# Kernel tuning notes

Measured on AMD Instinct MI355X. Metric: run time of the kernel, lower is better.

Reference implementation:

```python
import jax, jax.numpy as jnp
import numpy as np

DIM = 4096
NH = 32
NKV = 8
HD = DIM // NH          # 128
REP = NH // NKV          # 4
B = 1
T = 2048
THETA = 500000.0
NEG = -1e9


def setup_inputs() -> dict:
    key = jax.random.key(0)
    ks = jax.random.split(key, 6)
    x = jax.random.normal(ks[0], (B, T, DIM), jnp.float32)
    # RoPE tables (real/imag parts of freqs_cis = exp(i * t * inv_freq))
    inv_freq = 1.0 / (THETA ** (np.arange(0, HD, 2, dtype=np.float32) / HD))  # (HD/2,)
    ang = np.outer(np.arange(T, dtype=np.float32), inv_freq)                  # (T, HD/2)
    freqs_cos = jnp.asarray(np.cos(ang), jnp.float32)
    freqs_sin = jnp.asarray(np.sin(ang), jnp.float32)
    # additive causal mask for prefill (pos=0): (T, T)
    mask = jnp.where(np.tril(np.ones((T, T), dtype=bool)), 0.0, NEG).astype(jnp.float32)
    cache_k = jnp.zeros((B, T, NKV, HD), jnp.float32)
    cache_v = jnp.zeros((B, T, NKV, HD), jnp.float32)
    s = 0.02
    wk_w = jax.random.normal(ks[1], (NKV * HD, DIM), jnp.float32) * s
    wk_b = jnp.zeros((NKV * HD,), jnp.float32)
    wv_w = jax.random.normal(ks[2], (NKV * HD, DIM), jnp.float32) * s
    wv_b = jnp.zeros((NKV * HD,), jnp.float32)
    wo_w = jax.random.normal(ks[3], (DIM, DIM), jnp.float32) * s
    wo_b = jnp.zeros((DIM,), jnp.float32)
    return dict(x=x, freqs_cos=freqs_cos, freqs_sin=freqs_sin, mask=mask,
                cache_k=cache_k, cache_v=cache_v,
                wk_w=wk_w, wk_b=wk_b, wv_w=wv_w, wv_b=wv_b,
                wo_w=wo_w, wo_b=wo_b, pos=0)


def _rope(t, cos, sin):
    # t: (B, T, H, HD); pairs (even, odd) form complex numbers
    tr = t.reshape(*t.shape[:-1], HD // 2, 2)
    re, im = tr[..., 0], tr[..., 1]
    c = cos[None, :, None, :]
    s = sin[None, :, None, :]
    out = jnp.stack([re * c - im * s, re * s + im * c], axis=-1)
    return out.reshape(t.shape)


def reference(x, freqs_cos, freqs_sin, mask, cache_k, cache_v,
              wk_w, wk_b, wv_w, wv_b, wo_w, wo_b, pos):
    Bx, Tx, D = x.shape
    # NOTE: faithful to source bug -- q projection uses wo (shared with output proj)
    q = x @ wo_w.T + wo_b                        # (B, T, D)
    k = x @ wk_w.T + wk_b                        # (B, T, NKV*HD)
    v = x @ wv_w.T + wv_b
    q = q.reshape(Bx, Tx, NH, HD)
    k = k.reshape(Bx, Tx, NKV, HD)
    v = v.reshape(Bx, Tx, NKV, HD)
    q = _rope(q, freqs_cos, freqs_sin)
    k = _rope(k, freqs_cos, freqs_sin)
    # KV-cache append then read back [:pos+T]
    ck = cache_k.at[:Bx, pos:pos + Tx].set(k)
    cv = cache_v.at[:Bx, pos:pos + Tx].set(v)
    k = ck[:Bx, :pos + Tx]
    v = cv[:Bx, :pos + Tx]
    # repeat_kv (GQA expansion)
    k = jnp.repeat(k, REP, axis=2)               # (B, S, NH, HD)
    v = jnp.repeat(v, REP, axis=2)
    scale = 1.0 / jnp.sqrt(jnp.float32(HD))
    scores = jnp.einsum('bqhd,bkhd->bhqk', q, k) * scale
    scores = scores + mask[None, None, :, :]
    p = jax.nn.softmax(scores.astype(jnp.float32), axis=-1)
    out = jnp.einsum('bhqk,bkhd->bqhd', p, v).reshape(Bx, Tx, D)
    return out @ wo_w.T + wo_b
```

## Files before the change

kernel.cpp:

```cpp
#include <hip/hip_runtime.h>
#include <stdint.h>
#include <stddef.h>

#define T_SEQ 2048
#define DIM   4096
#define NH    32
#define NKV   8
#define HD    128
#define KVD   (NKV*HD)

typedef __attribute__((ext_vector_type(8))) short short8;
typedef __attribute__((ext_vector_type(4))) float floatx4;

static __device__ __forceinline__ float bf2f(short u) {
    union { unsigned int i; float f; } c; c.i = ((unsigned int)(unsigned short)u) << 16; return c.f;
}
static __device__ __forceinline__ short f2bf(float f) {
    union { float f; unsigned int u; } c; c.f = f;
    unsigned int r = c.u + 0x7fff + ((c.u >> 16) & 1);
    return (short)(r >> 16);
}
static __device__ __forceinline__ short8 ld8_f2b(const float* p) {
    floatx4 a = *(const floatx4*)p;
    floatx4 b = *(const floatx4*)(p + 4);
    short8 r;
    r[0]=f2bf(a[0]); r[1]=f2bf(a[1]); r[2]=f2bf(a[2]); r[3]=f2bf(a[3]);
    r[4]=f2bf(b[0]); r[5]=f2bf(b[1]); r[6]=f2bf(b[2]); r[7]=f2bf(b[3]);
    return r;
}

#define GLD16(g, l) __builtin_amdgcn_global_load_lds( \
    (const __attribute__((address_space(1))) unsigned int*)(g), \
    (__attribute__((address_space(3))) unsigned int*)(l), 16, 0, 0)

template<int CTRL>
static __device__ __forceinline__ float dppf(float x) {
    return __int_as_float(__builtin_amdgcn_update_dpp(
        0, __float_as_int(x), CTRL, 0xf, 0xf, true));
}
static __device__ __forceinline__ float rowmax16(float x) {
    x = fmaxf(x, dppf<0xB1>(x));
    x = fmaxf(x, dppf<0x4E>(x));
    x = fmaxf(x, dppf<0x141>(x));
    x = fmaxf(x, dppf<0x140>(x));
    return x;
}
static __device__ __forceinline__ float rowsum16(float x) {
    x += dppf<0xB1>(x);
    x += dppf<0x4E>(x);
    x += dppf<0x141>(x);
    x += dppf<0x140>(x);
    return x;
}

__global__ __launch_bounds__(256)
void cvt_bf16(const float* __restrict__ x, const float* __restrict__ wk,
              const float* __restrict__ wv, const float* __restrict__ wo,
              short* __restrict__ xb, short* __restrict__ wkb,
              short* __restrict__ wvb, short* __restrict__ wob) {
    size_t i8 = ((size_t)blockIdx.x * 256 + threadIdx.x) * 8;
    const float* src; short* dst; size_t off;
    if (i8 < 8388608)        { src = x;  dst = xb;  off = i8; }
    else if (i8 < 12582912)  { src = wk; dst = wkb; off = i8 - 8388608; }
    else if (i8 < 16777216)  { src = wv; dst = wvb; off = i8 - 12582912; }
    else                     { src = wo; dst = wob; off = i8 - 16777216; }
    *(short8*)(dst + off) = ld8_f2b(src + off);
}

template<bool C_F32>
static __device__ __forceinline__
void gemm_core(const short* __restrict__ A, const short* __restrict__ B,
               const float* __restrict__ bias, void* __restrict__ Cp,
               int N, int K, int bm, int bn) {
    __shared__ short sA0[128*32];
    __shared__ short sA1[128*32];
    __shared__ short sB0[128*32];
    __shared__ short sB1[128*32];
    const int tid  = threadIdx.x;
    const int wave = tid >> 6, lane = tid & 63;
    const int l15  = lane & 15, lq = lane >> 4;
    const int wm   = (wave >> 1) * 64, wn = (wave & 1) * 64;

    floatx4 acc[4][4];
    #pragma unroll
    for (int i = 0; i < 4; i++)
        #pragma unroll
        for (int j = 0; j < 4; j++)
            acc[i][j] = (floatx4)(0.0f);

    const int c0 = tid, c1 = 256 + tid;
    const int r0 = c0 >> 2, k0 = (c0 & 3) * 8;
    const int r1 = c1 >> 2, k1 = (c1 & 3) * 8;
    const short* pA0 = A + (size_t)(bm + r0) * K + k0;
    const short* pA1 = A + (size_t)(bm + r1) * K + k1;
    const short* pB0 = B + (size_t)(bn + r0) * K + k0;
    const short* pB1 = B + (size_t)(bn + r1) * K + k1;

    auto stage = [&](short* dA, short* dB, int kt) {
        GLD16(pA0 + kt, dA + c0 * 8);
        GLD16(pA1 + kt, dA + c1 * 8);
        GLD16(pB0 + kt, dB + c0 * 8);
        GLD16(pB1 + kt, dB + c1 * 8);
    };
    auto compute = [&](const short* dA, const short* dB) {
        short8 af[4], bfr[4];
        #pragma unroll
        for (int mi = 0; mi < 4; mi++)
            af[mi] = *(const short8*)&dA[(wm + mi*16 + l15)*32 + lq*8];
        #pragma unroll
        for (int ni = 0; ni < 4; ni++)
            bfr[ni] = *(const short8*)&dB[(wn + ni*16 + l15)*32 + lq*8];
        #pragma unroll
        for (int mi = 0; mi < 4; mi++)
            #pragma unroll
            for (int ni = 0; ni < 4; ni++)
                acc[mi][ni] = __builtin_amdgcn_mfma_f32_16x16x32_bf16(af[mi], bfr[ni], acc[mi][ni], 0, 0, 0);
    };

    stage(sA0, sB0, 0);
    __syncthreads();

    const int nt = K >> 5;
    for (int t = 0; t < nt; t += 2) {
        stage(sA1, sB1, (t + 1) * 32);
        compute(sA0, sB0);
        __syncthreads();
        if (t + 2 < nt) stage(sA0, sB0, (t + 2) * 32);
        compute(sA1, sB1);
        __syncthreads();
    }

    #pragma unroll
    for (int ni = 0; ni < 4; ni++) {
        int col = bn + wn + ni*16 + l15;
        float bv = bias[col];
        #pragma unroll
        for (int mi = 0; mi < 4; mi++) {
            int row = bm + wm + mi*16 + lq*4;
            #pragma unroll
            for (int r = 0; r < 4; r++) {
                float v = acc[mi][ni][r] + bv;
                if (C_F32) ((float*)Cp)[(size_t)(row + r)*N + col] = v;
                else       ((short*)Cp)[(size_t)(row + r)*N + col] = f2bf(v);
            }
        }
    }
}

template<bool C_F32>
__global__ __launch_bounds__(256)
void gemm_bt(const short* __restrict__ A, const short* __restrict__ B,
             const float* __restrict__ bias, void* __restrict__ Cp,
             int N, int K) {
    gemm_core<C_F32>(A, B, bias, Cp, N, K, blockIdx.y * 128, blockIdx.x * 128);
}

__global__ __launch_bounds__(256)
void gemm_kv(const short* __restrict__ A,
             const short* __restrict__ Bk, const float* __restrict__ bk, short* __restrict__ Ck,
             const short* __restrict__ Bv, const float* __restrict__ bv, short* __restrict__ Cv) {
    const short* B = blockIdx.z ? Bv : Bk;
    const float* bias = blockIdx.z ? bv : bk;
    short* C = blockIdx.z ? Cv : Ck;
    gemm_core<false>(A, B, bias, C, KVD, DIM, blockIdx.y * 128, blockIdx.x * 128);
}

__global__ __launch_bounds__(256)
void rope_k(short* __restrict__ Q, short* __restrict__ Kc,
            const float* __restrict__ fc, const float* __restrict__ fs) {
    int idx = blockIdx.x * 256 + threadIdx.x;
    const int NQ = T_SEQ * NH  * (HD/2);
    const int NK = T_SEQ * NKV * (HD/2);
    short* base; int t, i; size_t off;
    if (idx < NQ) {
        i = idx & 63;
        int th = idx >> 6;
        t = th >> 5;
        off = (size_t)th * HD + i*2;
        base = Q;
    } else if (idx < NQ + NK) {
        int kidx = idx - NQ;
        i = kidx & 63;
        int th = kidx >> 6;
        t = th >> 3;
        off = (size_t)th * HD + i*2;
        base = Kc;
    } else return;
    float re = bf2f(base[off]), im = bf2f(base[off+1]);
    float c = fc[t*64 + i], s = fs[t*64 + i];
    base[off]   = f2bf(re*c - im*s);
    base[off+1] = f2bf(re*s + im*c);
}

__global__ __launch_bounds__(256)
void vtrans(const short* __restrict__ V, short* __restrict__ Vt) {
    __shared__ short sT[64*72];
    const int tid = threadIdx.x;
    const int bt = blockIdx.x, bd = blockIdx.y;
    #pragma unroll
    for (int i = 0; i < 2; i++) {
        int c = i*256 + tid;
        int r = c >> 3, c8 = (c & 7) * 8;
        *(short8*)&sT[r*72 + c8] = *(const short8*)(V + (size_t)(bt*64 + r)*KVD + bd*64 + c8);
    }
    __syncthreads();
    #pragma unroll
    for (int i = 0; i < 2; i++) {
        int c = i*256 + tid;
        int d = c >> 3, t8 = (c & 7) * 8;
        short8 o;
        #pragma unroll
        for (int j = 0; j < 8; j++) o[j] = sT[(t8 + j)*72 + d];
        *(short8*)(Vt + (size_t)(bd*64 + d)*T_SEQ + bt*64 + t8) = o;
    }
}

#define ROWK 136
#define ROWV 72

__global__ __launch_bounds__(256, 2)
void flash_attn(const short* __restrict__ Q, const short* __restrict__ Kc,
                const short* __restrict__ Vt, short* __restrict__ O) {
    __shared__ short sK[64*ROWK];
    __shared__ short sV[128*ROWV];
    __shared__ short sP[4*2048];
    const int tid  = threadIdx.x;
    const int wave = tid >> 6, lane = tid & 63;
    const int l15  = lane & 15, lq = lane >> 4;
    const int kvg  = blockIdx.y;
    const int qt   = (blockIdx.y < 4) ? (int)blockIdx.x : 63 - (int)blockIdx.x;
    const int hl   = wave;
    const int qb   = qt * 32;
    const float scale = 0.08838834764831845f;

    short8 qf[2][4];
    #pragma unroll
    for (int mi = 0; mi < 2; mi++)
        #pragma unroll
        for (int ks = 0; ks < 4; ks++)
            qf[mi][ks] = *(const short8*)(Q + (size_t)(qb + mi*16 + l15)*DIM
                                          + kvg*512 + hl*128 + ks*32 + lq*8);

    short* sPw = sP + wave*2048;

    float m_r[2][4], l_r[2][4];
    floatx4 o_acc[2][8];
    #pragma unroll
    for (int mi = 0; mi < 2; mi++) {
        #pragma unroll
        for (int r = 0; r < 4; r++) { m_r[mi][r] = -1e30f; l_r[mi][r] = 0.0f; }
        #pragma unroll
        for (int nd = 0; nd < 8; nd++) o_acc[mi][nd] = (floatx4)(0.0f);
    }

    const int ktmax = qt >> 1;
    for (int kt = 0; kt <= ktmax; kt++) {
        short8 kbuf[4], vbuf[4];
        #pragma unroll
        for (int i = 0; i < 4; i++) {
            int c = i*256 + tid;
            int r = c >> 4, c8 = (c & 15) * 8;
            kbuf[i] = *(const short8*)(Kc + (size_t)(kt*64 + r)*KVD + kvg*HD + c8);
            int rv = c >> 3, v8 = (c & 7) * 8;
            vbuf[i] = *(const short8*)(Vt + (size_t)(kvg*HD + rv)*T_SEQ + kt*64 + v8);
        }
        __syncthreads();
        #pragma unroll
        for (int i = 0; i < 4; i++) {
            int c = i*256 + tid;
            int r = c >> 4, c8 = (c & 15) * 8;
            *(short8*)&sK[r*ROWK + c8] = kbuf[i];
            int rv = c >> 3, v8 = (c & 7) * 8;
            *(short8*)&sV[rv*ROWV + v8] = vbuf[i];
        }
        __syncthreads();

        floatx4 s_acc[2][4];
        #pragma unroll
        for (int mi = 0; mi < 2; mi++)
            #pragma unroll
            for (int ni = 0; ni < 4; ni++) s_acc[mi][ni] = (floatx4)(0.0f);
        __builtin_amdgcn_s_setprio(1);
        #pragma unroll
        for (int ks = 0; ks < 4; ks++)
            #pragma unroll
            for (int ni = 0; ni < 4; ni++) {
                short8 kf = *(const short8*)&sK[(ni*16 + l15)*ROWK + ks*32 + lq*8];
                s_acc[0][ni] = __builtin_amdgcn_mfma_f32_16x16x32_bf16(qf[0][ks], kf, s_acc[0][ni], 0, 0, 0);
                s_acc[1][ni] = __builtin_amdgcn_mfma_f32_16x16x32_bf16(qf[1][ks], kf, s_acc[1][ni], 0, 0, 0);
            }
        __builtin_amdgcn_s_setprio(0);

        const bool last = (kt == ktmax);

        #pragma unroll
        for (int mi = 0; mi < 2; mi++) {
            float sv[4][4], mx[4];
            #pragma unroll
            for (int r = 0; r < 4; r++) mx[r] = -1e30f;
            #pragma unroll
            for (int ni = 0; ni < 4; ni++) {
                int col = kt*64 + ni*16 + l15;
                #pragma unroll
                for (int r = 0; r < 4; r++) {
                    float x = s_acc[mi][ni][r] * scale;
                    if (last) {
                        int row = qb + mi*16 + lq*4 + r;
                        x = (col <= row) ? x : -1e30f;
                    }
                    sv[ni][r] = x;
                    mx[r] = fmaxf(mx[r], x);
                }
            }
            #pragma unroll
            for (int r = 0; r < 4; r++) mx[r] = rowmax16(mx[r]);

            float g = fmaxf(fmaxf(mx[0] - m_r[mi][0], mx[1] - m_r[mi][1]),
                            fmaxf(mx[2] - m_r[mi][2], mx[3] - m_r[mi][3]));
            if (__any(g > 8.0f)) {
                #pragma unroll
                for (int r = 0; r < 4; r++) {
                    float mn = fmaxf(m_r[mi][r], mx[r]);
                    float a  = __expf(m_r[mi][r] - mn);
                    m_r[mi][r] = mn;
                    l_r[mi][r] *= a;
                    #pragma unroll
                    for (int nd = 0; nd < 8; nd++) o_acc[mi][nd][r] *= a;
                }
            }

            float rs[4] = {0.0f, 0.0f, 0.0f, 0.0f};
            #pragma unroll
            for (int ni = 0; ni < 4; ni++)
                #pragma unroll
                for (int r = 0; r < 4; r++) {
                    float p = __expf(sv[ni][r] - m_r[mi][r]);
                    sv[ni][r] = p;
                    rs[r] += p;
                }
            #pragma unroll
            for (int r = 0; r < 4; r++) {
                rs[r] = rowsum16(rs[r]);
                l_r[mi][r] += rs[r];
            }

            #pragma unroll
            for (int ni = 0; ni < 4; ni++)
                #pragma unroll
                for (int r = 0; r < 4; r++) {
                    int q = mi*16 + lq*4 + r, k = ni*16 + l15;
                    sPw[q*64 + (((k >> 3) ^ (q & 7))*8) + (k & 7)] = f2bf(sv[ni][r]);
                }
        }

        __builtin_amdgcn_s_setprio(1);
        #pragma unroll
        for (int ks = 0; ks < 2; ks++) {
            int kk = ks*32 + lq*8;
            short8 pf[2];
            #pragma unroll
            for (int mi = 0; mi < 2; mi++) {
                int q = mi*16 + l15;
                pf[mi] = *(const short8*)&sPw[q*64 + (((kk >> 3) ^ (q & 7))*8)];
            }
            #pragma unroll
            for (int nd = 0; nd < 8; nd++) {
                short8 vf = *(const short8*)&sV[(nd*16 + l15)*ROWV + kk];
                o_acc[0][nd] = __builtin_amdgcn_mfma_f32_16x16x32_bf16(pf[0], vf, o_acc[0][nd], 0, 0, 0);
                o_acc[1][nd] = __builtin_amdgcn_mfma_f32_16x16x32_bf16(pf[1], vf, o_acc[1][nd], 0, 0, 0);
            }
        }
        __builtin_amdgcn_s_setprio(0);
    }

    #pragma unroll
    for (int mi = 0; mi < 2; mi++)
        #pragma unroll
        for (int nd = 0; nd < 8; nd++) {
            int col = (kvg*4 + hl)*HD + nd*16 + l15;
            #pragma unroll
            for (int r = 0; r < 4; r++) {
                int row = qb + mi*16 + lq*4 + r;
                O[(size_t)row*DIM + col] = f2bf(o_acc[mi][nd][r] / l_r[mi][r]);
            }
        }
}

extern "C" void kernel_launch(void* const* d_in, const int* in_sizes, int n_in,
                              void* d_out, int out_size, void* d_ws, size_t ws_size,
                              hipStream_t stream) {
    const float* x    = (const float*)d_in[0];
    const float* fc   = (const float*)d_in[1];
    const float* fs   = (const float*)d_in[2];
    const float* wk_w = (const float*)d_in[6];
    const float* wk_b = (const float*)d_in[7];
    const float* wv_w = (const float*)d_in[8];
    const float* wv_b = (const float*)d_in[9];
    const float* wo_w = (const float*)d_in[10];
    const float* wo_b = (const float*)d_in[11];
    float* out = (float*)d_out;

    short* xb  = (short*)d_ws;
    short* wkb = xb  + 8388608;
    short* wvb = wkb + 4194304;
    short* wob = wvb + 4194304;
    short* Q   = wob + 16777216;
    short* K   = Q   + 8388608;
    short* V   = K   + 2097152;
    short* Vt  = V   + 2097152;
    short* AO  = Vt  + 2097152;

    cvt_bf16<<<dim3(16384), dim3(256), 0, stream>>>(x, wk_w, wv_w, wo_w, xb, wkb, wvb, wob);

    gemm_bt<false><<<dim3(32, 16), dim3(256), 0, stream>>>(xb, wob, wo_b, Q, DIM, DIM);
    gemm_kv<<<dim3(8, 16, 2), dim3(256), 0, stream>>>(xb, wkb, wk_b, K, wvb, wv_b, V);

    int nrope = T_SEQ*NH*(HD/2) + T_SEQ*NKV*(HD/2);
    rope_k<<<dim3((nrope + 255)/256), dim3(256), 0, stream>>>(Q, K, fc, fs);

    vtrans<<<dim3(32, 16), dim3(256), 0, stream>>>(V, Vt);

    flash_attn<<<dim3(64, 8), dim3(256), 0, stream>>>(Q, K, Vt, AO);

    gemm_bt<true><<<dim3(32, 16), dim3(256), 0, stream>>>(AO, wob, wo_b, out, DIM, DIM);
}
```

Before: 530.3 us.

## Double-buffer K/V tiles with direct global-to-LDS loads and fold softmax scale into Q

The flash attention kernel now keeps two K and two V LDS buffers and prefetches the next tile with direct global-to-LDS loads (GLD16) while computing on the current one. The padded rows are replaced by an XOR swizzle to avoid bank conflicts. The softmax scale and log2(e) are folded into Q during RoPE so the kernel can use exp2 and skip the per-element scale multiply. LDS use grows, which may limit occupancy at two blocks per CU, and Q is scaled before bf16 rounding, which slightly changes numerics.

After: 519.0 us. 2.1% less time.

```diff
diff --git a/kernel.cpp b/kernel.cpp
--- a/kernel.cpp
+++ b/kernel.cpp
@@ -165,31 +165,33 @@
     gemm_core<false>(A, B, bias, C, KVD, DIM, blockIdx.y * 128, blockIdx.x * 128);
 }
 
+#define QSC (0.08838834764831845f * 1.4426950408889634f)
+
 __global__ __launch_bounds__(256)
 void rope_k(short* __restrict__ Q, short* __restrict__ Kc,
             const float* __restrict__ fc, const float* __restrict__ fs) {
     int idx = blockIdx.x * 256 + threadIdx.x;
     const int NQ = T_SEQ * NH  * (HD/2);
     const int NK = T_SEQ * NKV * (HD/2);
-    short* base; int t, i; size_t off;
+    short* base; int t, i; size_t off; float sc;
     if (idx < NQ) {
         i = idx & 63;
         int th = idx >> 6;
         t = th >> 5;
         off = (size_t)th * HD + i*2;
-        base = Q;
+        base = Q; sc = QSC;
     } else if (idx < NQ + NK) {
         int kidx = idx - NQ;
         i = kidx & 63;
         int th = kidx >> 6;
         t = th >> 3;
         off = (size_t)th * HD + i*2;
-        base = Kc;
+        base = Kc; sc = 1.0f;
     } else return;
     float re = bf2f(base[off]), im = bf2f(base[off+1]);
     float c = fc[t*64 + i], s = fs[t*64 + i];
-    base[off]   = f2bf(re*c - im*s);
-    base[off+1] = f2bf(re*s + im*c);
+    base[off]   = f2bf((re*c - im*s)*sc);
+    base[off+1] = f2bf((re*s + im*c)*sc);
 }
 
 __global__ __launch_bounds__(256)
@@ -215,23 +217,22 @@
     }
 }
 
-#define ROWK 136
-#define ROWV 72
-
 __global__ __launch_bounds__(256, 2)
 void flash_attn(const short* __restrict__ Q, const short* __restrict__ Kc,
                 const short* __restrict__ Vt, short* __restrict__ O) {
-    __shared__ short sK[64*ROWK];
-    __shared__ short sV[128*ROWV];
+    __shared__ short sK0[64*128];
+    __shared__ short sK1[64*128];
+    __shared__ short sV0[128*64];
+    __shared__ short sV1[128*64];
     __shared__ short sP[4*2048];
     const int tid  = threadIdx.x;
     const int wave = tid >> 6, lane = tid & 63;
     const int l15  = lane & 15, lq = lane >> 4;
+    const int sw   = l15 & 7;
     const int kvg  = blockIdx.y;
     const int qt   = (blockIdx.y < 4) ? (int)blockIdx.x : 63 - (int)blockIdx.x;
     const int hl   = wave;
     const int qb   = qt * 32;
-    const float scale = 0.08838834764831845f;
 
     short8 qf[2][4];
     #pragma unroll
@@ -243,6 +244,26 @@
 
     short* sPw = sP + wave*2048;
 
+    int kc_r[4], kc_jg[4], vc_r[4], vc_jg[4];
+    #pragma unroll
+    for (int i = 0; i < 4; i++) {
+        int c = i*256 + tid;
+        kc_r[i]  = c >> 4;
+        kc_jg[i] = (c & 15) ^ (kc_r[i] & 7);
+        vc_r[i]  = c >> 3;
+        vc_jg[i] = (c & 7) ^ (vc_r[i] & 7);
+    }
+    auto stage = [&](short* dK, short* dV, int kt) {
+        #pragma unroll
+        for (int i = 0; i < 4; i++) {
+            int c = i*256 + tid;
+            GLD16(Kc + (size_t)(kt*64 + kc_r[i])*KVD + kvg*HD + kc_jg[i]*8,
+                  dK + c*8);
+            GLD16(Vt + (size_t)(kvg*HD + vc_r[i])*T_SEQ + kt*64 + vc_jg[i]*8,
+                  dV + c*8);
+        }
+    };
+
     float m_r[2][4], l_r[2][4];
     floatx4 o_acc[2][8];
     #pragma unroll
@@ -254,26 +275,13 @@
     }
 
     const int ktmax = qt >> 1;
+    stage(sK0, sV0, 0);
+    __syncthreads();
+
     for (int kt = 0; kt <= ktmax; kt++) {
-        short8 kbuf[4], vbuf[4];
-        #pragma unroll
-        for (int i = 0; i < 4; i++) {
-            int c = i*256 + tid;
-            int r = c >> 4, c8 = (c & 15) * 8;
-            kbuf[i] = *(const short8*)(Kc + (size_t)(kt*64 + r)*KVD + kvg*HD + c8);
-            int rv = c >> 3, v8 = (c & 7) * 8;
-            vbuf[i] = *(const short8*)(Vt + (size_t)(kvg*HD + rv)*T_SEQ + kt*64 + v8);
-        }
-        __syncthreads();
-        #pragma unroll
-        for (int i = 0; i < 4; i++) {
-            int c = i*256 + tid;
-            int r = c >> 4, c8 = (c & 15) * 8;
-            *(short8*)&sK[r*ROWK + c8] = kbuf[i];
-            int rv = c >> 3, v8 = (c & 7) * 8;
-            *(short8*)&sV[rv*ROWV + v8] = vbuf[i];
-        }
-        __syncthreads();
+        short* bK = (kt & 1) ? sK1 : sK0;
+        short* bV = (kt & 1) ? sV1 : sV0;
+        if (kt < ktmax) stage((kt & 1) ? sK0 : sK1, (kt & 1) ? sV0 : sV1, kt + 1);
 
         floatx4 s_acc[2][4];
         #pragma unroll
@@ -285,7 +293,8 @@
         for (int ks = 0; ks < 4; ks++)
             #pragma unroll
             for (int ni = 0; ni < 4; ni++) {
-                short8 kf = *(const short8*)&sK[(ni*16 + l15)*ROWK + ks*32 + lq*8];
+                short8 kf = *(const short8*)&bK[(ni*16 + l15)*128
+                                                + (((ks*4 + lq) ^ sw)*8)];
                 s_acc[0][ni] = __builtin_amdgcn_mfma_f32_16x16x32_bf16(qf[0][ks], kf, s_acc[0][ni], 0, 0, 0);
                 s_acc[1][ni] = __builtin_amdgcn_mfma_f32_16x16x32_bf16(qf[1][ks], kf, s_acc[1][ni], 0, 0, 0);
             }
@@ -303,7 +312,7 @@
                 int col = kt*64 + ni*16 + l15;
                 #pragma unroll
                 for (int r = 0; r < 4; r++) {
-                    float x = s_acc[mi][ni][r] * scale;
+                    float x = s_acc[mi][ni][r];
                     if (last) {
                         int row = qb + mi*16 + lq*4 + r;
                         x = (col <= row) ? x : -1e30f;
@@ -321,7 +330,7 @@
                 #pragma unroll
                 for (int r = 0; r < 4; r++) {
                     float mn = fmaxf(m_r[mi][r], mx[r]);
-                    float a  = __expf(m_r[mi][r] - mn);
+                    float a  = __builtin_amdgcn_exp2f(m_r[mi][r] - mn);
                     m_r[mi][r] = mn;
                     l_r[mi][r] *= a;
                     #pragma unroll
@@ -334,7 +343,7 @@
             for (int ni = 0; ni < 4; ni++)
                 #pragma unroll
                 for (int r = 0; r < 4; r++) {
-                    float p = __expf(sv[ni][r] - m_r[mi][r]);
+                    float p = __builtin_amdgcn_exp2f(sv[ni][r] - m_r[mi][r]);
                     sv[ni][r] = p;
                     rs[r] += p;
                 }
@@ -365,12 +374,15 @@
             }
             #pragma unroll
             for (int nd = 0; nd < 8; nd++) {
-                short8 vf = *(const short8*)&sV[(nd*16 + l15)*ROWV + kk];
+                short8 vf = *(const short8*)&bV[(nd*16 + l15)*64
+                                                + (((ks*4 + lq) ^ sw)*8)];
                 o_acc[0][nd] = __builtin_amdgcn_mfma_f32_16x16x32_bf16(pf[0], vf, o_acc[0][nd], 0, 0, 0);
                 o_acc[1][nd] = __builtin_amdgcn_mfma_f32_16x16x32_bf16(pf[1], vf, o_acc[1][nd], 0, 0, 0);
             }
         }
         __builtin_amdgcn_s_setprio(0);
+
+        __syncthreads();
     }
 
     #pragma unroll
```
